# Kernel optimization log

Measured on AMD Instinct MI355X. Metric: run time of the kernel, lower is better.

The kernel has to match this reference:

```python
import jax, jax.numpy as jnp
import numpy as np

B, S, E = 2, 2048, 1024
H, HKV = 16, 4
D = E // H          # head_dim = 64
REP = H // HKV      # kv repeat factor = 4


def setup_inputs() -> dict:
    key = jax.random.key(0)
    ks = jax.random.split(key, 9)
    std = 0.02
    x = jax.random.normal(ks[0], (B, S, E), dtype=jnp.float32)
    # causal mask: True means masked (upper triangle, strictly above diagonal)
    mask = jnp.triu(jnp.ones((S, S), dtype=bool), k=1)
    wq_w = jax.random.normal(ks[1], (E, E), dtype=jnp.float32) * std
    wq_b = jax.random.normal(ks[2], (E,), dtype=jnp.float32) * std
    wk_w = jax.random.normal(ks[3], (HKV * D, E), dtype=jnp.float32) * std
    wk_b = jax.random.normal(ks[4], (HKV * D,), dtype=jnp.float32) * std
    wv_w = jax.random.normal(ks[5], (HKV * D, E), dtype=jnp.float32) * std
    wv_b = jax.random.normal(ks[6], (HKV * D,), dtype=jnp.float32) * std
    wo_w = jax.random.normal(ks[7], (E, E), dtype=jnp.float32) * std
    wo_b = jax.random.normal(ks[8], (E,), dtype=jnp.float32) * std
    return {"x": x, "mask": mask, "wq_w": wq_w, "wq_b": wq_b,
            "wk_w": wk_w, "wk_b": wk_b, "wv_w": wv_w, "wv_b": wv_b,
            "wo_w": wo_w, "wo_b": wo_b}


def reference(x, mask, wq_w, wq_b, wk_w, wk_b, wv_w, wv_b, wo_w, wo_b):
    b, s, e = x.shape
    # projections (torch Linear: x @ W.T + b)
    q = x @ wq_w.T + wq_b                       # [B,S,E]
    k = x @ wk_w.T + wk_b                       # [B,S,HKV*D]
    v = x @ wv_w.T + wv_b
    # q grouped by kv head: [B, HKV, REP, S, D]; k/v: [B, HKV, S, D]
    q = q.reshape(b, s, HKV, REP, D).transpose(0, 2, 3, 1, 4)
    k = k.reshape(b, s, HKV, D).transpose(0, 2, 1, 3)
    v = v.reshape(b, s, HKV, D).transpose(0, 2, 1, 3)
    scale = D ** (-0.5)
    # scores [B, HKV, REP, Sq, Skv] -- same math as physical repeat_kv
    scores = jnp.einsum('bgrsd,bgtd->bgrst', q, k) * scale
    scores = jnp.where(mask, -jnp.inf, scores)
    w = jax.nn.softmax(scores, axis=-1)
    ctx = jnp.einsum('bgrst,bgtd->bgrsd', w, v)  # [B,HKV,REP,S,D]
    ctx = ctx.transpose(0, 3, 1, 2, 4).reshape(b, s, e)
    return ctx @ wo_w.T + wo_b
```

## Files before the change

kernel.cpp:

```cpp
#include <hip/hip_runtime.h>


typedef __attribute__((ext_vector_type(8))) short bh8;
typedef __attribute__((ext_vector_type(4))) short sh4;
typedef __attribute__((ext_vector_type(4))) float fv4;
typedef __attribute__((ext_vector_type(2))) unsigned int uv2;

#define MFMA16 __builtin_amdgcn_mfma_f32_16x16x32_bf16

static __device__ __forceinline__ float fast_exp2(float x) {
  return __builtin_amdgcn_exp2f(x);
}
static __device__ __forceinline__ unsigned short f2bf(float f) {
  unsigned int u; __builtin_memcpy(&u, &f, 4);
  u += 0x7fffu + ((u >> 16) & 1u);
  return (unsigned short)(u >> 16);
}
static __device__ __forceinline__ unsigned int pack2(float a, float b) {
  unsigned int r;
  asm("v_cvt_pk_bf16_f32 %0, %1, %2" : "=v"(r) : "v"(a), "v"(b));
  return r;
}
static __device__ __forceinline__ void gload16(const short* g, short* l) {
  __builtin_amdgcn_global_load_lds(
      (const __attribute__((address_space(1))) void*)g,
      (__attribute__((address_space(3))) void*)l, 16, 0, 0);
}

static __device__ __forceinline__ bh8 pshuf(const float* p, int quad, int l16) {
  unsigned int u01 = pack2(p[0], p[1]);
  unsigned int u23 = pack2(p[2], p[3]);
  unsigned int u45 = pack2(p[4], p[5]);
  unsigned int u67 = pack2(p[6], p[7]);
  const int g0 = (((quad << 1)    ) & 3) * 16 + l16;
  const int g1 = (((quad << 1) + 1) & 3) * 16 + l16;
  unsigned int w0l = __shfl((int)u01, g0), w0h = __shfl((int)u45, g0);
  unsigned int w1l = __shfl((int)u23, g0), w1h = __shfl((int)u67, g0);
  unsigned int w2l = __shfl((int)u01, g1), w2h = __shfl((int)u45, g1);
  unsigned int w3l = __shfl((int)u23, g1), w3h = __shfl((int)u67, g1);
  const bool up = (quad & 2) != 0;
  union { unsigned int w[4]; bh8 v; } pu;
  pu.w[0] = up ? w0h : w0l;
  pu.w[1] = up ? w1h : w1l;
  pu.w[2] = up ? w2h : w2l;
  pu.w[3] = up ? w3h : w3l;
  return pu.v;
}

__global__ __launch_bounds__(256) void cvt_all(
    const float* __restrict__ x,  const float* __restrict__ wq,
    const float* __restrict__ wk, const float* __restrict__ wv,
    const float* __restrict__ wo,
    short* __restrict__ xb, short* __restrict__ wqkvb, short* __restrict__ wob)
{
  const int i = blockIdx.x * 256 + threadIdx.x;
  const float* src; short* dst; int j;
  if (i < 1048576)      { j = i;           src = x;  dst = xb; }
  else if (i < 1310720) { j = i - 1048576; src = wq; dst = wqkvb; }
  else if (i < 1376256) { j = i - 1310720; src = wk; dst = wqkvb + (size_t)1024 * 1024; }
  else if (i < 1441792) { j = i - 1376256; src = wv; dst = wqkvb + (size_t)1280 * 1024; }
  else                  { j = i - 1441792; src = wo; dst = wob; }
  const float4 v = ((const float4*)src)[j];
  sh4 o = { (short)f2bf(v.x), (short)f2bf(v.y),
            (short)f2bf(v.z), (short)f2bf(v.w) };
  ((sh4*)dst)[j] = o;
}

__global__ __launch_bounds__(256) void gemm_dbuf(
    const short* __restrict__ A, const short* __restrict__ W,
    const float* __restrict__ biasQ, const float* __restrict__ biasK,
    const float* __restrict__ biasV,
    short* __restrict__ Cq, short* __restrict__ Ck, short* __restrict__ Cvt,
    float* __restrict__ Cf,
    int M, int K, int S, int mode, float scaleQ)
{
  __shared__ short As[2][128 * 64];
  __shared__ short Bs[2][64 * 64];
  const int tid  = threadIdx.x;
  const int wave = tid >> 6, lane = tid & 63;
  const int quad = lane >> 4, l16 = lane & 15;
  const int row0 = blockIdx.x * 128, col0 = blockIdx.y * 64;
  const int wr = (wave >> 1) * 64, wc = (wave & 1) * 32;

  fv4 acc[4][2] = {};

  const int srow = lane >> 3;
  const int scg  = (lane & 7) ^ srow;
  const short* ag = A + (size_t)(row0 + wave * 32 + srow) * K + scg * 8;
  const short* bg = W + (size_t)(col0 + wave * 16 + srow) * K + scg * 8;

  auto stage = [&](int b, int k0) {
    #pragma unroll
    for (int e = 0; e < 4; e++)
      gload16(ag + (size_t)(e * 8) * K + k0, &As[b][(wave * 32 + e * 8) * 64]);
    #pragma unroll
    for (int e = 0; e < 2; e++)
      gload16(bg + (size_t)(e * 8) * K + k0, &Bs[b][(wave * 16 + e * 8) * 64]);
  };

  stage(0, 0);
  __syncthreads();
  const int nIter = K / 64;
  for (int it = 0; it < nIter; it++) {
    const int cur = it & 1;
    if (it + 1 < nIter) stage(cur ^ 1, (it + 1) * 64);

    #pragma unroll
    for (int kk = 0; kk < 2; kk++) {
      const int g = kk * 4 + quad;
      bh8 af[4], bf[2];
      #pragma unroll
      for (int i = 0; i < 4; i++) {
        const int r = wr + i * 16 + l16;
        af[i] = *(const bh8*)&As[cur][r * 64 + ((g ^ (r & 7)) * 8)];
      }
      #pragma unroll
      for (int j = 0; j < 2; j++) {
        const int r = wc + j * 16 + l16;
        bf[j] = *(const bh8*)&Bs[cur][r * 64 + ((g ^ (r & 7)) * 8)];
      }
      #pragma unroll
      for (int i = 0; i < 4; i++)
        #pragma unroll
        for (int j = 0; j < 2; j++)
          acc[i][j] = MFMA16(af[i], bf[j], acc[i][j], 0, 0, 0);
    }
    __syncthreads();
  }

  if (mode == 2) {
    float bv[2];
    #pragma unroll
    for (int j = 0; j < 2; j++) bv[j] = biasQ[col0 + wc + j * 16 + l16];
    #pragma unroll
    for (int i = 0; i < 4; i++) {
      const int row = row0 + wr + i * 16 + quad * 4;
      #pragma unroll
      for (int j = 0; j < 2; j++) {
        const int col = col0 + wc + j * 16 + l16;
        #pragma unroll
        for (int r = 0; r < 4; r++)
          Cf[(size_t)(row + r) * 1024 + col] = acc[i][j][r] + bv[j];
      }
    }
  } else if (col0 < 1024) {
    float bv[2];
    #pragma unroll
    for (int j = 0; j < 2; j++) bv[j] = biasQ[col0 + wc + j * 16 + l16];
    #pragma unroll
    for (int i = 0; i < 4; i++) {
      const int row = row0 + wr + i * 16 + quad * 4;
      #pragma unroll
      for (int j = 0; j < 2; j++) {
        const int col = col0 + wc + j * 16 + l16;
        #pragma unroll
        for (int r = 0; r < 4; r++)
          Cq[(size_t)(row + r) * 1024 + col] =
              (short)f2bf((acc[i][j][r] + bv[j]) * scaleQ);
      }
    }
  } else if (col0 < 1280) {
    float bv[2];
    #pragma unroll
    for (int j = 0; j < 2; j++) bv[j] = biasK[col0 + wc + j * 16 + l16 - 1024];
    #pragma unroll
    for (int i = 0; i < 4; i++) {
      const int row = row0 + wr + i * 16 + quad * 4;
      #pragma unroll
      for (int j = 0; j < 2; j++) {
        const int col = col0 + wc + j * 16 + l16 - 1024;
        #pragma unroll
        for (int r = 0; r < 4; r++)
          Ck[(size_t)(row + r) * 256 + col] = (short)f2bf(acc[i][j][r] + bv[j]);
      }
    }
  } else {
    float bv[2];
    #pragma unroll
    for (int j = 0; j < 2; j++) bv[j] = biasV[col0 + wc + j * 16 + l16 - 1280];
    const int b  = row0 / S;
    const int sb = row0 - b * S;
    #pragma unroll
    for (int i = 0; i < 4; i++) {
      const int s = sb + wr + i * 16 + quad * 4;
      #pragma unroll
      for (int j = 0; j < 2; j++) {
        const int np = col0 + wc + j * 16 + l16 - 1280;
        sh4 v = { (short)f2bf(acc[i][j][0] + bv[j]),
                  (short)f2bf(acc[i][j][1] + bv[j]),
                  (short)f2bf(acc[i][j][2] + bv[j]),
                  (short)f2bf(acc[i][j][3] + bv[j]) };
        *(sh4*)(Cvt + ((size_t)(b * 256 + np)) * S + s) = v;
      }
    }
  }
}

__global__ __launch_bounds__(256) void gqa_attn(
    const short* __restrict__ Q,
    const short* __restrict__ Kg,
    const short* __restrict__ Vt,
    short* __restrict__ ctx)
{
  const int S = 2048, E = 1024, KVE = 256;
  __shared__ short Ks[2][4096];
  __shared__ short Vs[2][4096];
  __shared__ short P2[4][16 * 64];

  const int wave = threadIdx.x >> 6;
  const int lane = threadIdx.x & 63;
  const int quad = lane >> 4, l16 = lane & 15;
  const int bh = blockIdx.y;
  const int b = bh >> 4, h = bh & 15, kv = h >> 2;

  const short* Kb = Kg + (size_t)b * S * KVE + kv * 64;
  const short* Vb = Vt + ((size_t)(b * 4 + kv)) * 64 * S;
  short* Pw = &P2[wave][0];

  const int srow = lane >> 3;
  const int scg  = (lane & 7) ^ srow;

  const int kc0 = (quad ^ (l16 & 7)) * 8;
  const int kc1 = ((quad ^ 4) ^ (l16 & 7)) * 8;
  const int l7  = l16 & 7;
  const int pwr = l16 * 64;
  const int prA = pwr + ((quad ^ l7) * 8);
  const int prB = pwr + (((4 + quad) ^ l7) * 8);

  auto stageKV = [&](int buf, int t0) {
    #pragma unroll
    for (int e = 0; e < 2; e++) {
      const int g = wave * 2 + e;
      const int row = g * 8 + srow;
      gload16(Kb + (size_t)(t0 + row) * KVE + scg * 8, &Ks[buf][g * 512]);
      gload16(Vb + (size_t)row * S + t0 + scg * 8,     &Vs[buf][g * 512]);
    }
  };

  for (int ph = 0; ph < 2; ph++) {
    const int j = ph ? (31 - (int)blockIdx.x) : (int)blockIdx.x;
    const int qblk0 = j * 64;
    const int q0 = qblk0 + wave * 16;

    const short* qrow = Q + (size_t)(b * S + q0 + l16) * E + h * 64 + quad * 8;
    bh8 qf0 = *(const bh8*)(qrow);
    bh8 qf1 = *(const bh8*)(qrow + 32);

    fv4 acc0{}, acc1{}, acc2{}, acc3{};
    float rs = 0.f;

    const int nInt = qblk0 >> 6;
    if (nInt > 0) {
      stageKV(0, 0);
      for (int it = 0; it < nInt; it++) {
        const int cur = it & 1;
        if (it + 1 < nInt) {
          stageKV(cur ^ 1, (it + 1) * 64);
          asm volatile("s_waitcnt vmcnt(4)" ::: "memory");
        } else {
          asm volatile("s_waitcnt vmcnt(0)" ::: "memory");
        }
        __builtin_amdgcn_sched_barrier(0);
        __builtin_amdgcn_s_barrier();

        fv4 st[4] = {};
        __builtin_amdgcn_s_setprio(1);
        #pragma unroll
        for (int i = 0; i < 4; i++) {
          const int tb = (i * 16 + l16) * 64;
          bh8 k0 = *(const bh8*)&Ks[cur][tb + kc0];
          bh8 k1 = *(const bh8*)&Ks[cur][tb + kc1];
          st[i] = MFMA16(k0, qf0, st[i], 0, 0, 0);
          st[i] = MFMA16(k1, qf1, st[i], 0, 0, 0);
        }
        __builtin_amdgcn_s_setprio(0);
        #pragma unroll
        for (int i = 0; i < 4; i++) {
          float p0 = fast_exp2(st[i][0]);
          float p1 = fast_exp2(st[i][1]);
          float p2 = fast_exp2(st[i][2]);
          float p3 = fast_exp2(st[i][3]);
          rs += (p0 + p1) + (p2 + p3);
          uv2 u = { pack2(p0, p1), pack2(p2, p3) };
          const int pg = ((i * 2 + (quad >> 1)) ^ l7) * 8 + (quad & 1) * 4;
          *(uv2*)&Pw[pwr + pg] = u;
        }
        bh8 pfA = *(const bh8*)&Pw[prA];
        bh8 pfB = *(const bh8*)&Pw[prB];
        __builtin_amdgcn_s_setprio(1);
        #pragma unroll
        for (int dt = 0; dt < 4; dt++) {
          const int db = (dt * 16 + l16) * 64;
          bh8 v0 = *(const bh8*)&Vs[cur][db + kc0];
          bh8 v1 = *(const bh8*)&Vs[cur][db + kc1];
          fv4* a = dt == 0 ? &acc0 : dt == 1 ? &acc1 : dt == 2 ? &acc2 : &acc3;
          *a = MFMA16(v0, pfA, *a, 0, 0, 0);
          *a = MFMA16(v1, pfB, *a, 0, 0, 0);
        }
        __builtin_amdgcn_s_setprio(0);
        asm volatile("s_waitcnt lgkmcnt(0)" ::: "memory");
        __builtin_amdgcn_sched_barrier(0);
        __builtin_amdgcn_s_barrier();
      }
    }

    const int nk = q0 + 16;
    for (int t0 = qblk0; t0 < nk; t0 += 32) {
      fv4 st0{}, st1{};
      {
        const short* kr = Kb + (size_t)(t0 + l16) * KVE + quad * 8;
        bh8 k0 = *(const bh8*)(kr);
        bh8 k1 = *(const bh8*)(kr + 32);
        st0 = MFMA16(k0, qf0, st0, 0, 0, 0);
        st0 = MFMA16(k1, qf1, st0, 0, 0, 0);
      }
      const bool do2 = (t0 + 16) < nk;
      if (do2) {
        const short* kr = Kb + (size_t)(t0 + 16 + l16) * KVE + quad * 8;
        bh8 k0 = *(const bh8*)(kr);
        bh8 k1 = *(const bh8*)(kr + 32);
        st1 = MFMA16(k0, qf0, st1, 0, 0, 0);
        st1 = MFMA16(k1, qf1, st1, 0, 0, 0);
      }
      const int qg = q0 + l16;
      float p[8];
      #pragma unroll
      for (int r = 0; r < 4; r++) {
        const int t = t0 + quad * 4 + r;
        p[r]     = (t <= qg)               ? fast_exp2(st0[r]) : 0.f;
        p[4 + r] = (do2 && (t + 16) <= qg) ? fast_exp2(st1[r]) : 0.f;
      }
      #pragma unroll
      for (int i = 0; i < 8; i++) rs += p[i];

      bh8 pf = pshuf(p, quad, l16);
      const short* vr = Vb + (size_t)l16 * S + t0 + quad * 8;
      acc0 = MFMA16(*(const bh8*)(vr),          pf, acc0, 0, 0, 0);
      acc1 = MFMA16(*(const bh8*)(vr + 16 * S), pf, acc1, 0, 0, 0);
      acc2 = MFMA16(*(const bh8*)(vr + 32 * S), pf, acc2, 0, 0, 0);
      acc3 = MFMA16(*(const bh8*)(vr + 48 * S), pf, acc3, 0, 0, 0);
    }

    float lsum = rs;
    lsum += __shfl_xor(lsum, 16);
    lsum += __shfl_xor(lsum, 32);
    const float inv = 1.f / lsum;

    short* orow = ctx + (size_t)(b * S + q0 + l16) * E + h * 64 + quad * 4;
    sh4 o0 = { (short)f2bf(acc0[0] * inv), (short)f2bf(acc0[1] * inv),
               (short)f2bf(acc0[2] * inv), (short)f2bf(acc0[3] * inv) };
    sh4 o1 = { (short)f2bf(acc1[0] * inv), (short)f2bf(acc1[1] * inv),
               (short)f2bf(acc1[2] * inv), (short)f2bf(acc1[3] * inv) };
    sh4 o2 = { (short)f2bf(acc2[0] * inv), (short)f2bf(acc2[1] * inv),
               (short)f2bf(acc2[2] * inv), (short)f2bf(acc2[3] * inv) };
    sh4 o3 = { (short)f2bf(acc3[0] * inv), (short)f2bf(acc3[1] * inv),
               (short)f2bf(acc3[2] * inv), (short)f2bf(acc3[3] * inv) };
    *(sh4*)(orow)      = o0;
    *(sh4*)(orow + 16) = o1;
    *(sh4*)(orow + 32) = o2;
    *(sh4*)(orow + 48) = o3;
  }
}

extern "C" void kernel_launch(void* const* d_in, const int* in_sizes, int n_in,
                              void* d_out, int out_size, void* d_ws, size_t ws_size,
                              hipStream_t stream)
{
  const float* x    = (const float*)d_in[0];
  const float* wq_w = (const float*)d_in[2];
  const float* wq_b = (const float*)d_in[3];
  const float* wk_w = (const float*)d_in[4];
  const float* wk_b = (const float*)d_in[5];
  const float* wv_w = (const float*)d_in[6];
  const float* wv_b = (const float*)d_in[7];
  const float* wo_w = (const float*)d_in[8];
  const float* wo_b = (const float*)d_in[9];
  float* out = (float*)d_out;

  const int S = 2048, E = 1024, M = 2 * S;
  const float sl2e = 0.125f * 1.44269504f;

  char* ob = (char*)d_out;
  short* Qb   = (short*)(ob);
  short* Kbuf = (short*)(ob + (size_t)( 8 << 20));
  short* Vtb  = (short*)(ob + (size_t)(10 << 20));

  char* ws = (char*)d_ws;
  short* xb    = (short*)(ws);
  short* wqkvb = (short*)(ws + (size_t)( 8 << 20));
  short* wob   = (short*)(ws + (size_t)(11 << 20));
  short* Cx    = xb;

  dim3 blk(256);
  cvt_all<<<dim3(6656), blk, 0, stream>>>(x, wq_w, wk_w, wv_w, wo_w,
                                          xb, wqkvb, wob);
  gemm_dbuf<<<dim3(M / 128, 1536 / 64), blk, 0, stream>>>(
      xb, wqkvb, wq_b, wk_b, wv_b, Qb, Kbuf, Vtb, nullptr, M, E, S, 0, sl2e);
  gqa_attn<<<dim3(16, 2 * 16), blk, 0, stream>>>(Qb, Kbuf, Vtb, Cx);
  gemm_dbuf<<<dim3(M / 128, 1024 / 64), blk, 0, stream>>>(
      Cx, wob, wo_b, nullptr, nullptr, nullptr, nullptr, nullptr, out,
      M, E, S, 2, 1.f);
}
```

Before: 172.4 us.

## Process 128-key tiles per iteration with interleaved QK/PV subtiles in attention

```diff
diff --git a/kernel.cpp b/kernel.cpp
--- a/kernel.cpp
+++ b/kernel.cpp
@@ -203,9 +203,9 @@
     short* __restrict__ ctx)
 {
   const int S = 2048, E = 1024, KVE = 256;
-  __shared__ short Ks[2][4096];
-  __shared__ short Vs[2][4096];
-  __shared__ short P2[4][16 * 64];
+  __shared__ short Ks[2][2][4096];
+  __shared__ short Vs[2][2][4096];
+  __shared__ short P2[4][2][1024];
 
   const int wave = threadIdx.x >> 6;
   const int lane = threadIdx.x & 63;
@@ -215,7 +215,8 @@
 
   const short* Kb = Kg + (size_t)b * S * KVE + kv * 64;
   const short* Vb = Vt + ((size_t)(b * 4 + kv)) * 64 * S;
-  short* Pw = &P2[wave][0];
+  short* PhA = &P2[wave][0][0];
+  short* PhB = &P2[wave][1][0];
 
   const int srow = lane >> 3;
   const int scg  = (lane & 7) ^ srow;
@@ -227,13 +228,13 @@
   const int prA = pwr + ((quad ^ l7) * 8);
   const int prB = pwr + (((4 + quad) ^ l7) * 8);
 
-  auto stageKV = [&](int buf, int t0) {
+  auto stage64 = [&](int buf, int half, int t0) {
     #pragma unroll
     for (int e = 0; e < 2; e++) {
       const int g = wave * 2 + e;
       const int row = g * 8 + srow;
-      gload16(Kb + (size_t)(t0 + row) * KVE + scg * 8, &Ks[buf][g * 512]);
-      gload16(Vb + (size_t)row * S + t0 + scg * 8,     &Vs[buf][g * 512]);
+      gload16(Kb + (size_t)(t0 + row) * KVE + scg * 8, &Ks[buf][half][g * 512]);
+      gload16(Vb + (size_t)row * S + t0 + scg * 8,     &Vs[buf][half][g * 512]);
     }
   };
 
@@ -249,13 +250,60 @@
     fv4 acc0{}, acc1{}, acc2{}, acc3{};
     float rs = 0.f;
 
-    const int nInt = qblk0 >> 6;
-    if (nInt > 0) {
-      stageKV(0, 0);
-      for (int it = 0; it < nInt; it++) {
+    auto qk_sub = [&](const short* ks, fv4* st) {
+      __builtin_amdgcn_s_setprio(1);
+      #pragma unroll
+      for (int i = 0; i < 4; i++) {
+        const int tb = (i * 16 + l16) * 64;
+        bh8 k0 = *(const bh8*)&ks[tb + kc0];
+        bh8 k1 = *(const bh8*)&ks[tb + kc1];
+        st[i] = MFMA16(k0, qf0, st[i], 0, 0, 0);
+        st[i] = MFMA16(k1, qf1, st[i], 0, 0, 0);
+      }
+      __builtin_amdgcn_s_setprio(0);
+    };
+    auto exppack = [&](fv4* st, short* Ph) {
+      #pragma unroll
+      for (int i = 0; i < 4; i++) {
+        float p0 = fast_exp2(st[i][0]);
+        float p1 = fast_exp2(st[i][1]);
+        float p2 = fast_exp2(st[i][2]);
+        float p3 = fast_exp2(st[i][3]);
+        rs += (p0 + p1) + (p2 + p3);
+        uv2 u = { pack2(p0, p1), pack2(p2, p3) };
+        const int pg = ((i * 2 + (quad >> 1)) ^ l7) * 8 + (quad & 1) * 4;
+        *(uv2*)&Ph[pwr + pg] = u;
+      }
+    };
+    auto pv_sub = [&](const short* vs, const short* Ph) {
+      bh8 pfA = *(const bh8*)&Ph[prA];
+      bh8 pfB = *(const bh8*)&Ph[prB];
+      __builtin_amdgcn_s_setprio(1);
+      #pragma unroll
+      for (int dt = 0; dt < 4; dt++) {
+        const int db = (dt * 16 + l16) * 64;
+        bh8 v0 = *(const bh8*)&vs[db + kc0];
+        bh8 v1 = *(const bh8*)&vs[db + kc1];
+        fv4* a = dt == 0 ? &acc0 : dt == 1 ? &acc1 : dt == 2 ? &acc2 : &acc3;
+        *a = MFMA16(v0, pfA, *a, 0, 0, 0);
+        *a = MFMA16(v1, pfB, *a, 0, 0, 0);
+      }
+      __builtin_amdgcn_s_setprio(0);
+    };
+
+    const int n64  = qblk0 >> 6;
+    const int n128 = n64 >> 1, rem = n64 & 1;
+    if (n64 > 0) {
+      stage64(0, 0, 0);
+      if (n128 > 0) stage64(0, 1, 64);
+      for (int it = 0; it < n128; it++) {
         const int cur = it & 1;
-        if (it + 1 < nInt) {
-          stageKV(cur ^ 1, (it + 1) * 64);
+        if (it + 1 < n128) {
+          stage64(cur ^ 1, 0, (it + 1) * 128);
+          stage64(cur ^ 1, 1, (it + 1) * 128 + 64);
+          asm volatile("s_waitcnt vmcnt(8)" ::: "memory");
+        } else if (rem) {
+          stage64(cur ^ 1, 0, n128 * 128);
           asm volatile("s_waitcnt vmcnt(4)" ::: "memory");
         } else {
           asm volatile("s_waitcnt vmcnt(0)" ::: "memory");
@@ -263,41 +311,27 @@
         __builtin_amdgcn_sched_barrier(0);
         __builtin_amdgcn_s_barrier();
 
-        fv4 st[4] = {};
-        __builtin_amdgcn_s_setprio(1);
-        #pragma unroll
-        for (int i = 0; i < 4; i++) {
-          const int tb = (i * 16 + l16) * 64;
-          bh8 k0 = *(const bh8*)&Ks[cur][tb + kc0];
-          bh8 k1 = *(const bh8*)&Ks[cur][tb + kc1];
-          st[i] = MFMA16(k0, qf0, st[i], 0, 0, 0);
-          st[i] = MFMA16(k1, qf1, st[i], 0, 0, 0);
-        }
-        __builtin_amdgcn_s_setprio(0);
-        #pragma unroll
-        for (int i = 0; i < 4; i++) {
-          float p0 = fast_exp2(st[i][0]);
-          float p1 = fast_exp2(st[i][1]);
-          float p2 = fast_exp2(st[i][2]);
-          float p3 = fast_exp2(st[i][3]);
-          rs += (p0 + p1) + (p2 + p3);
-          uv2 u = { pack2(p0, p1), pack2(p2, p3) };
-          const int pg = ((i * 2 + (quad >> 1)) ^ l7) * 8 + (quad & 1) * 4;
-          *(uv2*)&Pw[pwr + pg] = u;
-        }
-        bh8 pfA = *(const bh8*)&Pw[prA];
-        bh8 pfB = *(const bh8*)&Pw[prB];
-        __builtin_amdgcn_s_setprio(1);
-        #pragma unroll
-        for (int dt = 0; dt < 4; dt++) {
-          const int db = (dt * 16 + l16) * 64;
-          bh8 v0 = *(const bh8*)&Vs[cur][db + kc0];
-          bh8 v1 = *(const bh8*)&Vs[cur][db + kc1];
-          fv4* a = dt == 0 ? &acc0 : dt == 1 ? &acc1 : dt == 2 ? &acc2 : &acc3;
-          *a = MFMA16(v0, pfA, *a, 0, 0, 0);
-          *a = MFMA16(v1, pfB, *a, 0, 0, 0);
-        }
-        __builtin_amdgcn_s_setprio(0);
+        fv4 stA[4] = {}, stB[4] = {};
+        qk_sub(&Ks[cur][0][0], stA);
+        exppack(stA, PhA);
+        qk_sub(&Ks[cur][1][0], stB);
+        pv_sub(&Vs[cur][0][0], PhA);
+        exppack(stB, PhB);
+        pv_sub(&Vs[cur][1][0], PhB);
+
+        asm volatile("s_waitcnt lgkmcnt(0)" ::: "memory");
+        __builtin_amdgcn_sched_barrier(0);
+        __builtin_amdgcn_s_barrier();
+      }
+      if (rem) {
+        const int cur2 = n128 & 1;
+        asm volatile("s_waitcnt vmcnt(0)" ::: "memory");
+        __builtin_amdgcn_sched_barrier(0);
+        __builtin_amdgcn_s_barrier();
+        fv4 stA[4] = {};
+        qk_sub(&Ks[cur2][0][0], stA);
+        exppack(stA, PhA);
+        pv_sub(&Vs[cur2][0][0], PhA);
         asm volatile("s_waitcnt lgkmcnt(0)" ::: "memory");
         __builtin_amdgcn_sched_barrier(0);
         __builtin_amdgcn_s_barrier();
```

Result: faster. 168.1 us, median of 2 (-2.5%).
